# Optimization experiments

Measured on AMD Instinct MI355X. Metric: run time of the kernel, lower is better.

## Reference

```python
import jax, jax.numpy as jnp
import numpy as np

DF = 2  # downsampling_factor

def _conv1x1(x, w, b):
    # x: [N,C,T,H,W], w: [O,C], b: [O]
    return jnp.einsum('ncthw,oc->nothw', x, w) + b[None, :, None, None, None]

def _avgpool(x):
    # AvgPool3d(kernel=(1,k,k), stride=(1,s,s), pad=(0,p,p)), count_include_pad=True
    k, s = DF + 1, DF
    p = (DF + 1) // 2
    summed = jax.lax.reduce_window(
        x, 0.0, jax.lax.add,
        window_dimensions=(1, 1, 1, k, k),
        window_strides=(1, 1, 1, s, s),
        padding=((0, 0), (0, 0), (0, 0), (p, p), (p, p)))
    return summed / float(k * k)

def _grid(T, Hd, Wd, t_scale):
    xg = jnp.arange(Wd, dtype=jnp.float32) / ((Wd - 1) * 0.25) - 2.0
    yg = jnp.arange(Hd, dtype=jnp.float32) / ((Hd - 1) * 0.5) - 1.0
    tg = (jnp.arange(T, dtype=jnp.float32) / ((T - 1) * 0.5) - 1.0) * t_scale
    return jnp.stack(jnp.meshgrid(tg, yg, xg, indexing='ij'), axis=0)  # [3,T,Hd,Wd]

def setup_inputs() -> dict:
    key = jax.random.key(0)
    ks = jax.random.split(key, 9)
    C, IC, OC = 256, 128, 256
    x = jax.random.normal(ks[0], (2, C, 4, 64, 64), dtype=jnp.float32)
    sc = 0.05
    return {
        'x': x,
        'theta_w': jax.random.normal(ks[1], (IC, C), jnp.float32) * sc,
        'theta_b': jax.random.normal(ks[2], (IC,), jnp.float32) * sc,
        'phi_w': jax.random.normal(ks[3], (IC, C), jnp.float32) * sc,
        'phi_b': jax.random.normal(ks[4], (IC,), jnp.float32) * sc,
        'g_w': jax.random.normal(ks[5], (IC, C), jnp.float32) * sc,
        'g_b': jax.random.normal(ks[6], (IC,), jnp.float32) * sc,
        'W_w': jax.random.normal(ks[7], (OC, IC + 3), jnp.float32) * sc,
        'W_b': jax.random.normal(ks[8], (OC,), jnp.float32) * sc,
    }

def reference(x, theta_w, theta_b, phi_w, phi_b, g_w, g_b, W_w, W_b):
    N, C, T, H, W = x.shape
    IC = theta_w.shape[0]
    theta_x = _conv1x1(x, theta_w, theta_b)                       # [N,IC,T,H,W]
    theta_x = theta_x.transpose(0, 2, 3, 4, 1).reshape(N, T * H * W, IC)
    phi_x = _avgpool(_conv1x1(x, phi_w, phi_b))                   # [N,IC,T,Hd,Wd]
    Hd, Wd = phi_x.shape[-2], phi_x.shape[-1]
    phi_x = phi_x.reshape(N, IC, T * Hd * Wd)
    f_x = jax.nn.softmax(jnp.matmul(theta_x, phi_x), axis=-1)     # [N,THW,THdWd]
    g_x = _avgpool(_conv1x1(x, g_w, g_b))                         # [N,IC,T,Hd,Wd]
    grid = _grid(T, Hd, Wd, 0.1)                                   # [3,T,Hd,Wd]
    g_x = jnp.concatenate(
        [g_x, jnp.broadcast_to(grid[None], (N, 3, T, Hd, Wd))], axis=1)
    g_x = g_x.transpose(0, 2, 3, 4, 1).reshape(N, T * Hd * Wd, IC + 3)
    y = jnp.matmul(f_x, g_x)                                       # [N,THW,IC+3]
    y = y.transpose(0, 2, 1).reshape(N, IC + 3, T, H, W)
    return _conv1x1(y, W_w, W_b)
```

## Files before the change

kernel.cpp:

```cpp
#include <hip/hip_runtime.h>
#include <stdint.h>

typedef short short8 __attribute__((ext_vector_type(8)));
typedef float floatx4 __attribute__((ext_vector_type(4)));
typedef float floatx16 __attribute__((ext_vector_type(16)));
typedef unsigned uint4v __attribute__((ext_vector_type(4)));

#define MFMA16(a, b, c) __builtin_amdgcn_mfma_f32_16x16x32_bf16((a), (b), (c), 0, 0, 0)
#define MFMA32(a, b, c) __builtin_amdgcn_mfma_f32_32x32x16_bf16((a), (b), (c), 0, 0, 0)

#define SPLITS 3
#define CHUNK_BYTES 40960
#define CHUNK_SHORTS 20480
#define VOFF_SHORTS 8704

typedef __attribute__((address_space(1))) const void* gas1_cp;
typedef __attribute__((address_space(3))) void* las3_p;

__device__ __forceinline__ void gload_lds16(const void* g, void* l) {
    __builtin_amdgcn_global_load_lds((gas1_cp)g, (las3_p)l, 16, 0, 0);
}

__device__ __forceinline__ unsigned short f2bf(float f) {
    union { float f; unsigned u; } v; v.f = f;
    unsigned u = v.u;
    unsigned r = (u + 0x7FFFu + ((u >> 16) & 1u)) >> 16;
    return (unsigned short)r;
}
__device__ __forceinline__ unsigned short us(float f) {
    return (unsigned short)((__float_as_uint(f) + 0x8000u) >> 16);
}
__device__ __forceinline__ unsigned pkfast(float lo, float hi) {
    unsigned a = __float_as_uint(lo) + 0x8000u;
    unsigned b = __float_as_uint(hi) + 0x8000u;
    return __builtin_amdgcn_perm(b, a, 0x07060302u);
}

__global__ void k_prep(const float* th, const float* ph, const float* gw, const float* Ww,
                       unsigned short* TW, unsigned short* PW, unsigned short* GW,
                       unsigned short* Wp) {
    int i = blockIdx.x * 256 + threadIdx.x;
    if (i < 32768) {
        TW[i] = f2bf(th[i]);
    } else if (i < 65536) {
        PW[i - 32768] = f2bf(ph[i - 32768]);
    } else if (i < 98304) {
        GW[i - 65536] = f2bf(gw[i - 65536]);
    } else if (i < 98304 + 256 * 160) {
        int j = i - 98304;
        int oc = j / 160, k = j - oc * 160;
        Wp[j] = (k < 131) ? f2bf(Ww[oc * 131 + k]) : (unsigned short)0;
    }
}

__launch_bounds__(256)
__global__ void k_xt(const float* __restrict__ x, unsigned short* __restrict__ xT) {
    __shared__ unsigned short Xs[64][40];
    int tid = threadIdx.x;
    int n = blockIdx.y;
    int px0 = (blockIdx.x & 255) * 64;
    int c0 = (blockIdx.x >> 8) * 32;
    #pragma unroll
    for (int p = 0; p < 2; ++p) {
        int c = c0 + p * 16 + (tid >> 4);
        int l = tid & 15;
        const float* src = x + (((size_t)(n * 256 + c)) << 14) + px0 + 4 * l;
        float4 v = *(const float4*)src;
        int cc = c - c0;
        Xs[4 * l + 0][cc] = us(v.x);
        Xs[4 * l + 1][cc] = us(v.y);
        Xs[4 * l + 2][cc] = us(v.z);
        Xs[4 * l + 3][cc] = us(v.w);
    }
    __syncthreads();
    int px = tid >> 2, c8 = (tid & 3) * 8;
    short8 row = *(const short8*)&Xs[px][c8];
    *(short8*)(xT + (((size_t)n << 14) + px0 + px) * 256 + c0 + c8) = row;
}

__launch_bounds__(256)
__global__ void k_poolT(const float* __restrict__ x, unsigned short* __restrict__ xpT) {
    __shared__ unsigned short P[32][40];
    int tid = threadIdx.x;
    int n = blockIdx.y;
    int r = blockIdx.x & 127;
    int c0 = (blockIdx.x >> 7) * 32;
    int t = r >> 5, hd = r & 31;
    int wd = tid & 31;
    int cg = (tid >> 5) * 4;
    int h0 = 2 * hd - 1, w0 = 2 * wd - 1;
    #pragma unroll
    for (int jj = 0; jj < 4; ++jj) {
        int c = c0 + cg + jj;
        const float* base = x + (((size_t)(n * 256 + c) * 4 + t) << 12);
        float s = 0.f;
        #pragma unroll
        for (int dh = 0; dh < 3; ++dh) {
            int h = h0 + dh;
            if ((unsigned)h < 64u) {
                const float* row = base + h * 64;
                #pragma unroll
                for (int dw = 0; dw < 3; ++dw) {
                    int w = w0 + dw;
                    if ((unsigned)w < 64u) s += row[w];
                }
            }
        }
        P[wd][cg + jj] = us(s * (1.f / 9.f));
    }
    __syncthreads();
    int key = r * 32 + (tid >> 3);
    int cc = (tid & 7) * 4;
    uint2 w = *(const uint2*)&P[tid >> 3][cc];
    *(uint2*)(xpT + (((size_t)n << 12) + key) * 256 + c0 + cc) = w;
}

__launch_bounds__(256)
__global__ void k_convq(const unsigned short* __restrict__ xT, const unsigned short* __restrict__ TW,
                        const float* __restrict__ tb, unsigned short* __restrict__ Q) {
    __shared__ unsigned short Qs[4][16][132];
    int tid = threadIdx.x, wid = tid >> 6, lane = tid & 63, quad = lane >> 4, l16 = lane & 15;
    int n = blockIdx.y;
    int px0 = blockIdx.x * 64 + wid * 16;
    const unsigned short* xb = xT + (((size_t)n << 14) + px0 + l16) * 256;
    floatx4 acc[8];
    #pragma unroll
    for (int i = 0; i < 8; ++i) acc[i] = (floatx4)0.f;
    for (int kc = 0; kc < 8; ++kc) {
        int cbase = kc * 32 + quad * 8;
        short8 b = *(const short8*)(xb + cbase);
        #pragma unroll
        for (int mt = 0; mt < 8; ++mt) {
            short8 a = *(const short8*)(TW + (mt * 16 + l16) * 256 + cbase);
            acc[mt] = MFMA16(a, b, acc[mt]);
        }
    }
    #pragma unroll
    for (int mt = 0; mt < 8; ++mt) {
        int ic = mt * 16 + quad * 4;
        uint2 w;
        w.x = pkfast(acc[mt][0] + tb[ic], acc[mt][1] + tb[ic + 1]);
        w.y = pkfast(acc[mt][2] + tb[ic + 2], acc[mt][3] + tb[ic + 3]);
        *(uint2*)&Qs[wid][l16][ic] = w;
    }
    #pragma unroll
    for (int i = 0; i < 4; ++i) {
        int pxl = i * 4 + quad;
        short8 row = *(const short8*)&Qs[wid][pxl][l16 * 8];
        *(short8*)(Q + ((((size_t)n << 14) + px0 + pxl) << 7) + l16 * 8) = row;
    }
}

__launch_bounds__(256)
__global__ void k_convkv(const unsigned short* __restrict__ xpT,
                         const unsigned short* __restrict__ PW, const float* __restrict__ pb,
                         const unsigned short* __restrict__ GW, const float* __restrict__ gb,
                         unsigned short* __restrict__ Stg) {
    __shared__ unsigned short Ks[2][16][132];
    __shared__ unsigned short Vs[32][132];
    int tid = threadIdx.x, wid = tid >> 6, lane = tid & 63, quad = lane >> 4, l16 = lane & 15;
    int n = blockIdx.y;
    int c32 = blockIdx.x;
    int chunk = c32 >> 1, half = c32 & 1;
    int k0 = c32 * 32;
    int role = wid >> 1, kg = wid & 1;
    int key = k0 + kg * 16 + l16;
    unsigned short* sc = Stg + (size_t)(n * 64 + chunk) * CHUNK_SHORTS;
    const unsigned short* xb = xpT + (((size_t)n << 12) + key) * 256;
    const unsigned short* W = role ? GW : PW;
    const float* bias = role ? gb : pb;
    floatx4 acc[8];
    #pragma unroll
    for (int i = 0; i < 8; ++i) acc[i] = (floatx4)0.f;
    for (int kc = 0; kc < 8; ++kc) {
        int cbase = kc * 32 + quad * 8;
        short8 b = *(const short8*)(xb + cbase);
        #pragma unroll
        for (int mt = 0; mt < 8; ++mt) {
            short8 a = *(const short8*)(W + (mt * 16 + l16) * 256 + cbase);
            acc[mt] = MFMA16(a, b, acc[mt]);
        }
    }
    int hd = (key >> 5) & 31, wdd = key & 31;
    float frac = ((hd == 0) ? 2.f : 3.f) * ((wdd == 0) ? 2.f : 3.f) * (1.f / 9.f);

    if (role == 0) {
        #pragma unroll
        for (int mt = 0; mt < 8; ++mt) {
            int ic = mt * 16 + quad * 4;
            uint2 w;
            w.x = pkfast(acc[mt][0] + bias[ic] * frac, acc[mt][1] + bias[ic + 1] * frac);
            w.y = pkfast(acc[mt][2] + bias[ic + 2] * frac, acc[mt][3] + bias[ic + 3] * frac);
            *(uint2*)&Ks[kg][l16][ic] = w;
        }
        #pragma unroll
        for (int i = 0; i < 4; ++i) {
            int pxl = i * 4 + quad;
            short8 row = *(const short8*)&Ks[kg][pxl][l16 * 8];
            *(short8*)(sc + (half * 32 + kg * 16 + pxl) * 136 + l16 * 8) = row;
        }
    } else {
        #pragma unroll
        for (int mt = 0; mt < 8; ++mt) {
            int ic = mt * 16 + quad * 4;
            uint2 w;
            w.x = pkfast(acc[mt][0] + bias[ic] * frac, acc[mt][1] + bias[ic + 1] * frac);
            w.y = pkfast(acc[mt][2] + bias[ic + 2] * frac, acc[mt][3] + bias[ic + 3] * frac);
            *(uint2*)&Vs[kg * 16 + l16][ic] = w;
        }
    }
    __syncthreads();
    #pragma unroll
    for (int it2 = 0; it2 < 2; ++it2) {
        int ic = it2 * 64 + (tid >> 2);
        int kk = (tid & 3) * 8;
        uint4v w;
        #pragma unroll
        for (int j = 0; j < 4; ++j) {
            unsigned s0 = Vs[kk + 2 * j][ic];
            unsigned s1 = Vs[kk + 2 * j + 1][ic];
            w[j] = s0 | (s1 << 16);
        }
        *(uint4v*)(sc + VOFF_SHORTS + ic * 72 + half * 32 + kk) = w;
    }
    #pragma unroll
    for (int it = 0; it < 4; ++it) {
        int e = it * 256 + tid;
        int row = 128 + (e >> 5);
        int kl = e & 31;
        int kk = k0 + kl;
        int t = kk >> 10, hh = (kk >> 5) & 31, ww = kk & 31;
        unsigned short v = 0;
        if (row == 128) v = f2bf(((float)t * (1.f / 1.5f) - 1.f) * 0.1f);
        else if (row == 129) v = f2bf((float)hh * (1.f / 15.5f) - 1.f);
        else if (row == 130) v = f2bf((float)ww * (1.f / 7.75f) - 2.f);
        sc[VOFF_SHORTS + row * 72 + half * 32 + kl] = v;
    }
}

__device__ __forceinline__ void softmax_pv(const floatx16 st, int ks,
                                           const short (*Vlds)[72], floatx16* O,
                                           float& lacc, int l32, int half) {
    unsigned u[8];
    #pragma unroll
    for (int a = 0; a < 4; ++a) {
        float p0 = exp2f(fmaf(st[4 * a + 0], 1.44269504f, -17.3123404907f));
        float p1 = exp2f(fmaf(st[4 * a + 1], 1.44269504f, -17.3123404907f));
        float p2 = exp2f(fmaf(st[4 * a + 2], 1.44269504f, -17.3123404907f));
        float p3 = exp2f(fmaf(st[4 * a + 3], 1.44269504f, -17.3123404907f));
        lacc += (p0 + p1) + (p2 + p3);
        u[2 * a] = pkfast(p0, p1);
        u[2 * a + 1] = pkfast(p2, p3);
    }
    unsigned xu[8];
    #pragma unroll
    for (int g = 0; g < 8; ++g) xu[g] = (unsigned)__shfl_xor((int)u[g], 32);
    uint4v pw0, pw1;
    pw0[0] = half ? xu[2] : u[0];
    pw0[1] = half ? xu[3] : u[1];
    pw0[2] = half ? u[2] : xu[0];
    pw0[3] = half ? u[3] : xu[1];
    pw1[0] = half ? xu[6] : u[4];
    pw1[1] = half ? xu[7] : u[5];
    pw1[2] = half ? u[6] : xu[4];
    pw1[3] = half ? u[7] : xu[5];
    short8 pf0 = __builtin_bit_cast(short8, pw0);
    short8 pf1 = __builtin_bit_cast(short8, pw1);
    #pragma unroll
    for (int vt = 0; vt < 5; ++vt) {
        short8 vf0 = *(const short8*)&Vlds[vt * 32 + l32][ks * 32 + half * 8];
        O[vt] = MFMA32(vf0, pf0, O[vt]);
        short8 vf1 = *(const short8*)&Vlds[vt * 32 + l32][ks * 32 + 16 + half * 8];
        O[vt] = MFMA32(vf1, pf1, O[vt]);
    }
}

__launch_bounds__(256, 3)
__global__ void k_attn(const unsigned short* __restrict__ Q,
                       const unsigned char* __restrict__ Stg,
                       unsigned short* __restrict__ Y, float* __restrict__ L) {
    __shared__ __align__(16) char Sh[CHUNK_BYTES];
    int tid = threadIdx.x, wid = tid >> 6, lane = tid & 63;
    int l32 = lane & 31, half = lane >> 5;
    int n = blockIdx.y, sp = blockIdx.z;
    int c0 = (sp * 64) / SPLITS, c1 = ((sp + 1) * 64) / SPLITS;
    int nch = c1 - c0;
    int q0 = blockIdx.x * 128 + wid * 32;

    const unsigned short* Qr = Q + ((((size_t)n << 14) + q0 + l32) << 7);
    short8 qf[8];
    #pragma unroll
    for (int kc = 0; kc < 8; ++kc) qf[kc] = *(const short8*)(Qr + kc * 16 + half * 8);

    floatx16 O[5];
    #pragma unroll
    for (int t = 0; t < 5; ++t) O[t] = (floatx16)0.f;
    float lacc = 0.f;

    const short (*Klds)[136] = (const short(*)[136])Sh;
    const short (*Vlds)[72] = (const short(*)[72])(Sh + 17408);

    const unsigned char* gsl = Stg + ((size_t)(n * 64 + c0)) * CHUNK_BYTES
                               + (wid * 10) * 1024 + lane * 16;
    char* lsl = Sh + (wid * 10) * 1024;

    for (int it = 0; it < nch; ++it) {
        __syncthreads();
        const unsigned char* g = gsl + (size_t)it * CHUNK_BYTES;
        #pragma unroll
        for (int i = 0; i < 10; ++i)
            gload_lds16(g + i * 1024, lsl + i * 1024);
        asm volatile("s_waitcnt vmcnt(0)" ::: "memory");
        __syncthreads();

        #pragma unroll
        for (int ks = 0; ks < 2; ++ks) {
            floatx16 st = (floatx16)0.f;
            #pragma unroll
            for (int kc = 0; kc < 8; ++kc) {
                short8 kf = *(const short8*)&Klds[ks * 32 + l32][kc * 16 + half * 8];
                st = MFMA32(kf, qf[kc], st);
            }
            softmax_pv(st, ks, Vlds, O, lacc, l32, half);
        }
    }
    float lt = lacc + __shfl_xor(lacc, 32);
    int slab = sp * 2 + n;
    unsigned short* Yb = Y + ((((size_t)slab << 14) + q0 + l32) * 160);
    #pragma unroll
    for (int vt = 0; vt < 5; ++vt)
        #pragma unroll
        for (int g = 0; g < 4; ++g) {
            int vd = vt * 32 + 8 * g + 4 * half;
            uint2 w;
            w.x = pkfast(O[vt][4 * g], O[vt][4 * g + 1]);
            w.y = pkfast(O[vt][4 * g + 2], O[vt][4 * g + 3]);
            *(uint2*)(Yb + vd) = w;
        }
    if (lane < 32) L[(((size_t)slab) << 14) + q0 + lane] = lt;
}

__launch_bounds__(256)
__global__ void k_convf(const unsigned short* __restrict__ Y, const float* __restrict__ L,
                        const unsigned short* __restrict__ Wp, const float* __restrict__ Wb,
                        float* __restrict__ out) {
    int tid = threadIdx.x, wid = tid >> 6, lane = tid & 63, quad = lane >> 4, l16 = lane & 15;
    int n = blockIdx.y;
    int p0 = blockIdx.x * 64;
    floatx4 acc[4][4];
    #pragma unroll
    for (int i = 0; i < 4; ++i)
        #pragma unroll
        for (int j = 0; j < 4; ++j) acc[i][j] = (floatx4)0.f;
    for (int kc = 0; kc < 5; ++kc) {
        int cb = kc * 32 + quad * 8;
        short8 a[4];
        #pragma unroll
        for (int mt = 0; mt < 4; ++mt)
            a[mt] = *(const short8*)(Wp + (size_t)(wid * 64 + mt * 16 + l16) * 160 + cb);
        #pragma unroll
        for (int sp = 0; sp < SPLITS; ++sp) {
            const unsigned short* Yb = Y + ((((size_t)(sp * 2 + n)) << 14) + p0) * 160;
            #pragma unroll
            for (int nt = 0; nt < 4; ++nt) {
                short8 b = *(const short8*)(Yb + (size_t)(nt * 16 + l16) * 160 + cb);
                #pragma unroll
                for (int mt = 0; mt < 4; ++mt) acc[mt][nt] = MFMA16(a[mt], b, acc[mt][nt]);
            }
        }
    }
    float linv[4];
    #pragma unroll
    for (int nt = 0; nt < 4; ++nt) {
        int p = p0 + nt * 16 + l16;
        float ls = 0.f;
        #pragma unroll
        for (int sp = 0; sp < SPLITS; ++sp) ls += L[(((size_t)(sp * 2 + n)) << 14) + p];
        linv[nt] = 1.f / ls;
    }
    #pragma unroll
    for (int mt = 0; mt < 4; ++mt)
        #pragma unroll
        for (int r = 0; r < 4; ++r) {
            int oc = wid * 64 + mt * 16 + quad * 4 + r;
            float bb = Wb[oc];
            float* orow = out + ((((size_t)n << 8) + oc) << 14) + p0;
            #pragma unroll
            for (int nt = 0; nt < 4; ++nt)
                orow[nt * 16 + l16] = acc[mt][nt][r] * linv[nt] + bb;
        }
}

extern "C" void kernel_launch(void* const* d_in, const int* in_sizes, int n_in,
                              void* d_out, int out_size, void* d_ws, size_t ws_size,
                              hipStream_t stream) {
    (void)in_sizes; (void)n_in; (void)out_size; (void)ws_size;
    const float* x   = (const float*)d_in[0];
    const float* thw = (const float*)d_in[1];
    const float* thb = (const float*)d_in[2];
    const float* phw = (const float*)d_in[3];
    const float* phb = (const float*)d_in[4];
    const float* gw_ = (const float*)d_in[5];
    const float* gb_ = (const float*)d_in[6];
    const float* Ww  = (const float*)d_in[7];
    const float* Wb  = (const float*)d_in[8];
    float* out = (float*)d_out;

    char* ws = (char*)d_ws;
    size_t off = 0;
    auto alloc = [&](size_t b) { size_t o = off; off += (b + 255) & ~(size_t)255; return o; };
    unsigned short* TW = (unsigned short*)(ws + alloc(32768 * 2));
    unsigned short* PW = (unsigned short*)(ws + alloc(32768 * 2));
    unsigned short* GW = (unsigned short*)(ws + alloc(32768 * 2));
    unsigned short* Wp = (unsigned short*)(ws + alloc(40960 * 2));
    unsigned short* Qb = (unsigned short*)(ws + alloc((size_t)32768 * 128 * 2));
    unsigned short* St = (unsigned short*)(ws + alloc((size_t)2 * 64 * CHUNK_BYTES));
    float*          Lb = (float*)(ws + alloc((size_t)SPLITS * 2 * 16384 * 4));
    size_t ybytes = (size_t)SPLITS * 2 * 16384 * 160 * 2;
    unsigned short* Yb  = (unsigned short*)(ws + alloc(ybytes));
    unsigned short* xT  = Yb;
    unsigned short* xpT = (unsigned short*)((char*)Yb + (size_t)2 * 16384 * 256 * 2);

    k_prep<<<(139264 + 255) / 256, 256, 0, stream>>>(thw, phw, gw_, Ww, TW, PW, GW, Wp);
    k_xt<<<dim3(2048, 2), 256, 0, stream>>>(x, xT);
    k_poolT<<<dim3(1024, 2), 256, 0, stream>>>(x, xpT);
    k_convq<<<dim3(256, 2), 256, 0, stream>>>(xT, TW, thb, Qb);
    k_convkv<<<dim3(128, 2), 256, 0, stream>>>(xpT, PW, phb, GW, gb_, St);
    k_attn<<<dim3(128, 2, SPLITS), 256, 0, stream>>>(Qb, (const unsigned char*)St, Yb, Lb);
    k_convf<<<dim3(256, 2), 256, 0, stream>>>(Yb, Lb, Wp, Wb, out);
}
```

Before: 251.9 us.

## Fuse transpose and pooling into 1x1 convs; register-prefetch attention K/V chunks

The bf16 transpose kernel is merged into the query conv, and the avg-pool transpose kernel is merged into the key/value conv. Each now reads fp32 x directly and stages a 32-channel slice in LDS per step, so the xT/xpT intermediate buffers and two kernel launches go away. The attention kernel drops direct global-to-LDS loads and instead prefetches the next K/V chunk into registers while computing on the current one. Its launch bound is lowered to 2 blocks per SM to make room for the extra registers. The fused conv kernels add syncs per channel step and recompute the pooling in fewer blocks, which lowers parallelism.

```diff
diff --git a/kernel.cpp b/kernel.cpp
--- a/kernel.cpp
+++ b/kernel.cpp
@@ -13,13 +13,6 @@
 #define CHUNK_BYTES 40960
 #define CHUNK_SHORTS 20480
 #define VOFF_SHORTS 8704
-
-typedef __attribute__((address_space(1))) const void* gas1_cp;
-typedef __attribute__((address_space(3))) void* las3_p;
-
-__device__ __forceinline__ void gload_lds16(const void* g, void* l) {
-    __builtin_amdgcn_global_load_lds((gas1_cp)g, (las3_p)l, 16, 0, 0);
-}
 
 __device__ __forceinline__ unsigned short f2bf(float f) {
     union { float f; unsigned u; } v; v.f = f;
@@ -54,86 +47,39 @@
 }
 
 __launch_bounds__(256)
-__global__ void k_xt(const float* __restrict__ x, unsigned short* __restrict__ xT) {
-    __shared__ unsigned short Xs[64][40];
-    int tid = threadIdx.x;
-    int n = blockIdx.y;
-    int px0 = (blockIdx.x & 255) * 64;
-    int c0 = (blockIdx.x >> 8) * 32;
-    #pragma unroll
-    for (int p = 0; p < 2; ++p) {
-        int c = c0 + p * 16 + (tid >> 4);
-        int l = tid & 15;
-        const float* src = x + (((size_t)(n * 256 + c)) << 14) + px0 + 4 * l;
-        float4 v = *(const float4*)src;
-        int cc = c - c0;
-        Xs[4 * l + 0][cc] = us(v.x);
-        Xs[4 * l + 1][cc] = us(v.y);
-        Xs[4 * l + 2][cc] = us(v.z);
-        Xs[4 * l + 3][cc] = us(v.w);
-    }
-    __syncthreads();
-    int px = tid >> 2, c8 = (tid & 3) * 8;
-    short8 row = *(const short8*)&Xs[px][c8];
-    *(short8*)(xT + (((size_t)n << 14) + px0 + px) * 256 + c0 + c8) = row;
-}
-
-__launch_bounds__(256)
-__global__ void k_poolT(const float* __restrict__ x, unsigned short* __restrict__ xpT) {
-    __shared__ unsigned short P[32][40];
-    int tid = threadIdx.x;
-    int n = blockIdx.y;
-    int r = blockIdx.x & 127;
-    int c0 = (blockIdx.x >> 7) * 32;
-    int t = r >> 5, hd = r & 31;
-    int wd = tid & 31;
-    int cg = (tid >> 5) * 4;
-    int h0 = 2 * hd - 1, w0 = 2 * wd - 1;
-    #pragma unroll
-    for (int jj = 0; jj < 4; ++jj) {
-        int c = c0 + cg + jj;
-        const float* base = x + (((size_t)(n * 256 + c) * 4 + t) << 12);
-        float s = 0.f;
-        #pragma unroll
-        for (int dh = 0; dh < 3; ++dh) {
-            int h = h0 + dh;
-            if ((unsigned)h < 64u) {
-                const float* row = base + h * 64;
-                #pragma unroll
-                for (int dw = 0; dw < 3; ++dw) {
-                    int w = w0 + dw;
-                    if ((unsigned)w < 64u) s += row[w];
-                }
-            }
-        }
-        P[wd][cg + jj] = us(s * (1.f / 9.f));
-    }
-    __syncthreads();
-    int key = r * 32 + (tid >> 3);
-    int cc = (tid & 7) * 4;
-    uint2 w = *(const uint2*)&P[tid >> 3][cc];
-    *(uint2*)(xpT + (((size_t)n << 12) + key) * 256 + c0 + cc) = w;
-}
-
-__launch_bounds__(256)
-__global__ void k_convq(const unsigned short* __restrict__ xT, const unsigned short* __restrict__ TW,
-                        const float* __restrict__ tb, unsigned short* __restrict__ Q) {
-    __shared__ unsigned short Qs[4][16][132];
+__global__ void k_xtq(const float* __restrict__ x, const unsigned short* __restrict__ TW,
+                      const float* __restrict__ tb, unsigned short* __restrict__ Q) {
+    __shared__ __align__(16) char smem[16896];
+    unsigned short (*Xs)[40] = (unsigned short(*)[40])smem;
+    unsigned short (*Qs)[16][132] = (unsigned short(*)[16][132])smem;
     int tid = threadIdx.x, wid = tid >> 6, lane = tid & 63, quad = lane >> 4, l16 = lane & 15;
     int n = blockIdx.y;
-    int px0 = blockIdx.x * 64 + wid * 16;
-    const unsigned short* xb = xT + (((size_t)n << 14) + px0 + l16) * 256;
+    int px0 = blockIdx.x * 64;
     floatx4 acc[8];
     #pragma unroll
     for (int i = 0; i < 8; ++i) acc[i] = (floatx4)0.f;
-    for (int kc = 0; kc < 8; ++kc) {
-        int cbase = kc * 32 + quad * 8;
-        short8 b = *(const short8*)(xb + cbase);
+    for (int cc = 0; cc < 8; ++cc) {
+        int c0 = cc * 32;
+        #pragma unroll
+        for (int p = 0; p < 2; ++p) {
+            int c = c0 + p * 16 + (tid >> 4);
+            int l = tid & 15;
+            const float* src = x + (((size_t)(n * 256 + c)) << 14) + px0 + 4 * l;
+            float4 v = *(const float4*)src;
+            int ccl = c - c0;
+            Xs[4 * l + 0][ccl] = us(v.x);
+            Xs[4 * l + 1][ccl] = us(v.y);
+            Xs[4 * l + 2][ccl] = us(v.z);
+            Xs[4 * l + 3][ccl] = us(v.w);
+        }
+        __syncthreads();
+        short8 b = *(const short8*)&Xs[wid * 16 + l16][quad * 8];
         #pragma unroll
         for (int mt = 0; mt < 8; ++mt) {
-            short8 a = *(const short8*)(TW + (mt * 16 + l16) * 256 + cbase);
+            short8 a = *(const short8*)(TW + (mt * 16 + l16) * 256 + c0 + quad * 8);
             acc[mt] = MFMA16(a, b, acc[mt]);
         }
+        __syncthreads();
     }
     #pragma unroll
     for (int mt = 0; mt < 8; ++mt) {
@@ -147,15 +93,16 @@
     for (int i = 0; i < 4; ++i) {
         int pxl = i * 4 + quad;
         short8 row = *(const short8*)&Qs[wid][pxl][l16 * 8];
-        *(short8*)(Q + ((((size_t)n << 14) + px0 + pxl) << 7) + l16 * 8) = row;
+        *(short8*)(Q + ((((size_t)n << 14) + px0 + wid * 16 + pxl) << 7) + l16 * 8) = row;
     }
 }
 
 __launch_bounds__(256)
-__global__ void k_convkv(const unsigned short* __restrict__ xpT,
-                         const unsigned short* __restrict__ PW, const float* __restrict__ pb,
-                         const unsigned short* __restrict__ GW, const float* __restrict__ gb,
-                         unsigned short* __restrict__ Stg) {
+__global__ void k_pkv(const float* __restrict__ x,
+                      const unsigned short* __restrict__ PW, const float* __restrict__ pb,
+                      const unsigned short* __restrict__ GW, const float* __restrict__ gb,
+                      unsigned short* __restrict__ Stg) {
+    __shared__ unsigned short Ps[32][40];
     __shared__ unsigned short Ks[2][16][132];
     __shared__ unsigned short Vs[32][132];
     int tid = threadIdx.x, wid = tid >> 6, lane = tid & 63, quad = lane >> 4, l16 = lane & 15;
@@ -166,22 +113,45 @@
     int role = wid >> 1, kg = wid & 1;
     int key = k0 + kg * 16 + l16;
     unsigned short* sc = Stg + (size_t)(n * 64 + chunk) * CHUNK_SHORTS;
-    const unsigned short* xb = xpT + (((size_t)n << 12) + key) * 256;
     const unsigned short* W = role ? GW : PW;
     const float* bias = role ? gb : pb;
+    int t = c32 >> 5, hd = c32 & 31;
+    int wd = tid & 31, cg = (tid >> 5) * 4;
+    int h0 = 2 * hd - 1, w0 = 2 * wd - 1;
     floatx4 acc[8];
     #pragma unroll
     for (int i = 0; i < 8; ++i) acc[i] = (floatx4)0.f;
-    for (int kc = 0; kc < 8; ++kc) {
-        int cbase = kc * 32 + quad * 8;
-        short8 b = *(const short8*)(xb + cbase);
+    for (int cc = 0; cc < 8; ++cc) {
+        int c0 = cc * 32;
+        #pragma unroll
+        for (int jj = 0; jj < 4; ++jj) {
+            int c = c0 + cg + jj;
+            const float* base = x + (((size_t)(n * 256 + c) * 4 + t) << 12);
+            float s = 0.f;
+            #pragma unroll
+            for (int dh = 0; dh < 3; ++dh) {
+                int h = h0 + dh;
+                if ((unsigned)h < 64u) {
+                    const float* row = base + h * 64;
+                    #pragma unroll
+                    for (int dw = 0; dw < 3; ++dw) {
+                        int w = w0 + dw;
+                        if ((unsigned)w < 64u) s += row[w];
+                    }
+                }
+            }
+            Ps[wd][cg + jj] = us(s * (1.f / 9.f));
+        }
+        __syncthreads();
+        short8 b = *(const short8*)&Ps[kg * 16 + l16][quad * 8];
         #pragma unroll
         for (int mt = 0; mt < 8; ++mt) {
-            short8 a = *(const short8*)(W + (mt * 16 + l16) * 256 + cbase);
+            short8 a = *(const short8*)(W + (mt * 16 + l16) * 256 + c0 + quad * 8);
             acc[mt] = MFMA16(a, b, acc[mt]);
         }
-    }
-    int hd = (key >> 5) & 31, wdd = key & 31;
+        __syncthreads();
+    }
+    int wdd = key & 31;
     float frac = ((hd == 0) ? 2.f : 3.f) * ((wdd == 0) ? 2.f : 3.f) * (1.f / 9.f);
 
     if (role == 0) {
@@ -229,9 +199,9 @@
         int row = 128 + (e >> 5);
         int kl = e & 31;
         int kk = k0 + kl;
-        int t = kk >> 10, hh = (kk >> 5) & 31, ww = kk & 31;
+        int tt = kk >> 10, hh = (kk >> 5) & 31, ww = kk & 31;
         unsigned short v = 0;
-        if (row == 128) v = f2bf(((float)t * (1.f / 1.5f) - 1.f) * 0.1f);
+        if (row == 128) v = f2bf(((float)tt * (1.f / 1.5f) - 1.f) * 0.1f);
         else if (row == 129) v = f2bf((float)hh * (1.f / 15.5f) - 1.f);
         else if (row == 130) v = f2bf((float)ww * (1.f / 7.75f) - 2.f);
         sc[VOFF_SHORTS + row * 72 + half * 32 + kl] = v;
@@ -275,7 +245,7 @@
     }
 }
 
-__launch_bounds__(256, 3)
+__launch_bounds__(256, 2)
 __global__ void k_attn(const unsigned short* __restrict__ Q,
                        const unsigned char* __restrict__ Stg,
                        unsigned short* __restrict__ Y, float* __restrict__ L) {
@@ -302,16 +272,24 @@
 
     const unsigned char* gsl = Stg + ((size_t)(n * 64 + c0)) * CHUNK_BYTES
                                + (wid * 10) * 1024 + lane * 16;
-    char* lsl = Sh + (wid * 10) * 1024;
+    char* lsl = Sh + (wid * 10) * 1024 + lane * 16;
+
+    uint4v pf[10];
+    #pragma unroll
+    for (int i = 0; i < 10; ++i) pf[i] = *(const uint4v*)(gsl + i * 1024);
 
     for (int it = 0; it < nch; ++it) {
         __syncthreads();
-        const unsigned char* g = gsl + (size_t)it * CHUNK_BYTES;
         #pragma unroll
         for (int i = 0; i < 10; ++i)
-            gload_lds16(g + i * 1024, lsl + i * 1024);
-        asm volatile("s_waitcnt vmcnt(0)" ::: "memory");
-        __syncthreads();
+            *(uint4v*)(lsl + i * 1024) = pf[i];
+        __syncthreads();
+        if (it + 1 < nch) {
+            const unsigned char* g = gsl + (size_t)(it + 1) * CHUNK_BYTES;
+            #pragma unroll
+            for (int i = 0; i < 10; ++i) pf[i] = *(const uint4v*)(g + i * 1024);
+        }
+        __builtin_amdgcn_sched_barrier(0);
 
         #pragma unroll
         for (int ks = 0; ks < 2; ++ks) {
@@ -418,14 +396,10 @@
     float*          Lb = (float*)(ws + alloc((size_t)SPLITS * 2 * 16384 * 4));
     size_t ybytes = (size_t)SPLITS * 2 * 16384 * 160 * 2;
     unsigned short* Yb  = (unsigned short*)(ws + alloc(ybytes));
-    unsigned short* xT  = Yb;
-    unsigned short* xpT = (unsigned short*)((char*)Yb + (size_t)2 * 16384 * 256 * 2);
 
     k_prep<<<(139264 + 255) / 256, 256, 0, stream>>>(thw, phw, gw_, Ww, TW, PW, GW, Wp);
-    k_xt<<<dim3(2048, 2), 256, 0, stream>>>(x, xT);
-    k_poolT<<<dim3(1024, 2), 256, 0, stream>>>(x, xpT);
-    k_convq<<<dim3(256, 2), 256, 0, stream>>>(xT, TW, thb, Qb);
-    k_convkv<<<dim3(128, 2), 256, 0, stream>>>(xpT, PW, phb, GW, gb_, St);
+    k_xtq<<<dim3(256, 2), 256, 0, stream>>>(x, TW, thb, Qb);
+    k_pkv<<<dim3(128, 2), 256, 0, stream>>>(x, PW, phb, GW, gb_, St);
     k_attn<<<dim3(128, 2, SPLITS), 256, 0, stream>>>(Qb, (const unsigned char*)St, Yb, Lb);
     k_convf<<<dim3(256, 2), 256, 0, stream>>>(Yb, Lb, Wp, Wb, out);
 }
```

After: 275.9 us. 1.1x slower.

## Split K/V staging to overlap next-chunk loads with attention compute

Applied to the files above, without the earlier changes.

Restructures the attention main loop so K and V tiles for the next chunk are loaded asynchronously into LDS in separate phases. The K load overlaps the softmax·V work and the V load overlaps the next QK product, using explicit vmcnt waits, raw barriers and sched_barrier fences. It also lowers the KV split count from 3 to 2, giving fewer blocks with longer loops and a smaller partial-result combine. The risk is that a single shared LDS buffer is reused across phases, so correctness depends on the exact waitcnt and barrier ordering. Fewer splits also reduce parallelism.

```diff
diff --git a/kernel.cpp b/kernel.cpp
--- a/kernel.cpp
+++ b/kernel.cpp
@@ -9,7 +9,7 @@
 #define MFMA16(a, b, c) __builtin_amdgcn_mfma_f32_16x16x32_bf16((a), (b), (c), 0, 0, 0)
 #define MFMA32(a, b, c) __builtin_amdgcn_mfma_f32_32x32x16_bf16((a), (b), (c), 0, 0, 0)
 
-#define SPLITS 3
+#define SPLITS 2
 #define CHUNK_BYTES 40960
 #define CHUNK_SHORTS 20480
 #define VOFF_SHORTS 8704
@@ -275,6 +275,8 @@
     }
 }
 
+#define SFENCE() __builtin_amdgcn_sched_barrier(0)
+
 __launch_bounds__(256, 3)
 __global__ void k_attn(const unsigned short* __restrict__ Q,
                        const unsigned char* __restrict__ Stg,
@@ -300,30 +302,64 @@
     const short (*Klds)[136] = (const short(*)[136])Sh;
     const short (*Vlds)[72] = (const short(*)[72])(Sh + 17408);
 
-    const unsigned char* gsl = Stg + ((size_t)(n * 64 + c0)) * CHUNK_BYTES
-                               + (wid * 10) * 1024 + lane * 16;
-    char* lsl = Sh + (wid * 10) * 1024;
+    const unsigned char* gbase = Stg + ((size_t)(n * 64 + c0)) * CHUNK_BYTES;
+    int woff = wid << 10;
+    int lgo = woff + lane * 16;
+
+#define STAGE_K(gch) do { const unsigned char* g_ = (gch);                     \
+        gload_lds16(g_ + 0 * 4096 + lgo, Sh + 0 * 4096 + woff);                \
+        gload_lds16(g_ + 1 * 4096 + lgo, Sh + 1 * 4096 + woff);                \
+        gload_lds16(g_ + 2 * 4096 + lgo, Sh + 2 * 4096 + woff);                \
+        gload_lds16(g_ + 3 * 4096 + lgo, Sh + 3 * 4096 + woff);                \
+        gload_lds16(g_ + 13312 + lgo,    Sh + 13312 + woff); } while (0)
+#define STAGE_V(gch) do { const unsigned char* g_ = (gch);                     \
+        gload_lds16(g_ + 17408 + 0 * 4096 + lgo, Sh + 17408 + 0 * 4096 + woff);\
+        gload_lds16(g_ + 17408 + 1 * 4096 + lgo, Sh + 17408 + 1 * 4096 + woff);\
+        gload_lds16(g_ + 17408 + 2 * 4096 + lgo, Sh + 17408 + 2 * 4096 + woff);\
+        gload_lds16(g_ + 17408 + 3 * 4096 + lgo, Sh + 17408 + 3 * 4096 + woff);\
+        gload_lds16(g_ + 17408 + 4 * 4096 + lgo, Sh + 17408 + 4 * 4096 + woff);\
+        gload_lds16(g_ + 36864 + lgo,            Sh + 36864 + woff); } while (0)
+
+    STAGE_K(gbase);
+    STAGE_V(gbase);
+    SFENCE();
+    asm volatile("s_waitcnt vmcnt(6)" ::: "memory");
+    SFENCE();
+    __builtin_amdgcn_s_barrier();
+    SFENCE();
 
     for (int it = 0; it < nch; ++it) {
-        __syncthreads();
-        const unsigned char* g = gsl + (size_t)it * CHUNK_BYTES;
-        #pragma unroll
-        for (int i = 0; i < 10; ++i)
-            gload_lds16(g + i * 1024, lsl + i * 1024);
+        floatx16 st0 = (floatx16)0.f, st1 = (floatx16)0.f;
+        #pragma unroll
+        for (int kc = 0; kc < 8; ++kc) {
+            short8 kf0 = *(const short8*)&Klds[l32][kc * 16 + half * 8];
+            st0 = MFMA32(kf0, qf[kc], st0);
+            short8 kf1 = *(const short8*)&Klds[32 + l32][kc * 16 + half * 8];
+            st1 = MFMA32(kf1, qf[kc], st1);
+        }
+        SFENCE();
         asm volatile("s_waitcnt vmcnt(0)" ::: "memory");
-        __syncthreads();
-
-        #pragma unroll
-        for (int ks = 0; ks < 2; ++ks) {
-            floatx16 st = (floatx16)0.f;
-            #pragma unroll
-            for (int kc = 0; kc < 8; ++kc) {
-                short8 kf = *(const short8*)&Klds[ks * 32 + l32][kc * 16 + half * 8];
-                st = MFMA32(kf, qf[kc], st);
-            }
-            softmax_pv(st, ks, Vlds, O, lacc, l32, half);
-        }
-    }
+        SFENCE();
+        __builtin_amdgcn_s_barrier();
+        SFENCE();
+        if (it + 1 < nch) STAGE_K(gbase + (size_t)(it + 1) * CHUNK_BYTES);
+        softmax_pv(st0, 0, Vlds, O, lacc, l32, half);
+        softmax_pv(st1, 1, Vlds, O, lacc, l32, half);
+        SFENCE();
+        __builtin_amdgcn_s_barrier();
+        SFENCE();
+        if (it + 1 < nch) {
+            STAGE_V(gbase + (size_t)(it + 1) * CHUNK_BYTES);
+            SFENCE();
+            asm volatile("s_waitcnt vmcnt(6)" ::: "memory");
+            SFENCE();
+        }
+        __builtin_amdgcn_s_barrier();
+        SFENCE();
+    }
+#undef STAGE_K
+#undef STAGE_V
+
     float lt = lacc + __shfl_xor(lacc, 32);
     int slab = sp * 2 + n;
     unsigned short* Yb = Y + ((((size_t)slab << 14) + q0 + l32) * 160);
```

Measured after the change: 266.3 us. 5.7% more time.
